# Optimization experiments

Hardware: AMD Instinct MI355X
Metric: run time of the kernel (lower is better)

## Reference

```python
import jax, jax.numpy as jnp
import numpy as np

N, E, IN_DIM, HID = 100000, 1000000, 128, 64


def setup_inputs() -> dict:
    key = jax.random.key(0)
    ks = jax.random.split(key, 9)
    x = jax.random.normal(ks[0], (N, IN_DIM), dtype=jnp.float32)
    edge_index = jax.random.randint(ks[1], (2, E), 0, N, dtype=jnp.int32)
    edge_weight = jax.random.uniform(ks[2], (E,), dtype=jnp.float32)
    # GCNConv / Linear parameters (glorot-ish scaling)
    W1 = jax.random.normal(ks[3], (IN_DIM, HID), dtype=jnp.float32) / np.sqrt(IN_DIM)
    b1 = jnp.zeros((HID,), jnp.float32)
    W2 = jax.random.normal(ks[4], (HID, HID), dtype=jnp.float32) / np.sqrt(HID)
    b2 = jnp.zeros((HID,), jnp.float32)
    Wl = jax.random.normal(ks[5], (HID, 1), dtype=jnp.float32) / np.sqrt(HID)
    bl = jnp.zeros((1,), jnp.float32)
    return {"x": x, "edge_index": edge_index, "edge_weight": edge_weight,
            "W1": W1, "b1": b1, "W2": W2, "b2": b2, "Wl": Wl, "bl": bl}


def _propagate(h, src, dst, norm, num_nodes):
    # gather neighbor features, weight by norm, scatter-add to destinations
    msg = h[src] * norm[:, None]  # [E+N, HID]
    return jax.ops.segment_sum(msg, dst, num_segments=num_nodes)


def reference(x, edge_index, edge_weight, W1, b1, W2, b2, Wl, bl):
    n = x.shape[0]
    loop = jnp.arange(n, dtype=edge_index.dtype)
    # add self-loops with weight 1 (PyG GCNConv default)
    src = jnp.concatenate([edge_index[0], loop])
    dst = jnp.concatenate([edge_index[1], loop])
    ew = jnp.concatenate([edge_weight, jnp.ones((n,), x.dtype)])
    # symmetric normalization: D^-1/2 A D^-1/2
    deg = jax.ops.segment_sum(ew, dst, num_segments=n)
    dinv = jnp.where(deg > 0, jax.lax.rsqrt(deg), 0.0)
    norm = dinv[src] * ew * dinv[dst]  # [E+N]

    h = _propagate(x @ W1, src, dst, norm, n) + b1
    h = jax.nn.relu(h)  # dropout is identity in eval mode
    h = _propagate(h @ W2, src, dst, norm, n) + b2
    h = jax.nn.relu(h)
    return (h @ Wl + bl).squeeze(-1)  # [N]
```

## Files before the change

### kernel.cpp

```cpp
#include <hip/hip_runtime.h>

#define IN_DIM 128
#define HID    64
#define SCAN_B 256

typedef __attribute__((ext_vector_type(4))) _Float16 f16x4;
typedef __attribute__((ext_vector_type(8))) _Float16 f16x8;
typedef __attribute__((ext_vector_type(4))) float    f32x4;

__global__ void k_prep_w(const float* __restrict__ W1, const float* __restrict__ W2,
                         _Float16* __restrict__ W1T, _Float16* __restrict__ W2T) {
    int i = blockIdx.x * blockDim.x + threadIdx.x;
    if (i < IN_DIM * HID) { int k = i >> 6, c = i & 63; W1T[c * IN_DIM + k] = (_Float16)W1[i]; }
    if (i < HID * HID)    { int k = i >> 6, c = i & 63; W2T[c * HID + k]    = (_Float16)W2[i]; }
}

__global__ void k_hist_rank(const int* __restrict__ dst, int* __restrict__ counts,
                            int* __restrict__ rank, int e) {
    int i = blockIdx.x * blockDim.x + threadIdx.x;
    if (i < e) rank[i] = atomicAdd(&counts[dst[i]], 1);
}

__global__ __launch_bounds__(SCAN_B) void k_scan1(int* __restrict__ data,
                                                  int* __restrict__ blockSums, int n) {
    __shared__ int s[SCAN_B];
    int tid = threadIdx.x;
    int gid = blockIdx.x * SCAN_B + tid;
    int v = (gid < n) ? data[gid] : 0;
    s[tid] = v;
    __syncthreads();
    for (int off = 1; off < SCAN_B; off <<= 1) {
        int t = (tid >= off) ? s[tid - off] : 0;
        __syncthreads();
        s[tid] += t;
        __syncthreads();
    }
    if (gid < n) data[gid] = s[tid] - v;
    if (tid == SCAN_B - 1) blockSums[blockIdx.x] = s[tid];
}

__global__ __launch_bounds__(512) void k_scan2(int* __restrict__ blockSums, int nb) {
    __shared__ int s[512];
    int tid = threadIdx.x;
    int v = (tid < nb) ? blockSums[tid] : 0;
    s[tid] = v;
    __syncthreads();
    for (int off = 1; off < 512; off <<= 1) {
        int t = (tid >= off) ? s[tid - off] : 0;
        __syncthreads();
        s[tid] += t;
        __syncthreads();
    }
    if (tid < nb) blockSums[tid] = s[tid] - v;
}

__global__ __launch_bounds__(SCAN_B) void k_scan3(int* __restrict__ data,
                                                  const int* __restrict__ blockSums,
                                                  int n, int e) {
    int gid = blockIdx.x * SCAN_B + threadIdx.x;
    if (gid < n) {
        data[gid] += blockSums[blockIdx.x];
        if (gid == n - 1) data[n] = e;
    }
}

__global__ void k_scatter(const int* __restrict__ src, const int* __restrict__ dst,
                          const float* __restrict__ ew, const int* __restrict__ rank,
                          const int* __restrict__ rowOff, int2* __restrict__ sedge, int e) {
    int i = blockIdx.x * blockDim.x + threadIdx.x;
    if (i >= e) return;
    int pos = rowOff[dst[i]] + rank[i];
    sedge[pos] = make_int2(src[i], __float_as_int(ew[i]));
}

__global__ void k_deg_dinv(const int* __restrict__ rowOff, const int2* __restrict__ sedge,
                           float* __restrict__ dinv, int n) {
    int v = blockIdx.x * blockDim.x + threadIdx.x;
    if (v >= n) return;
    int s = rowOff[v], t = rowOff[v + 1];
    float a = 1.0f;
    for (int j = s; j < t; ++j) a += __int_as_float(sedge[j].y);
    dinv[v] = rsqrtf(a);
}


__global__ __launch_bounds__(256) void k_gemm1(const float* __restrict__ x,
                                               const _Float16* __restrict__ W1T,
                                               const float* __restrict__ dinv,
                                               _Float16* __restrict__ h0, int n) {
    __shared__ _Float16 sX[4][16 * IN_DIM];
    int tid  = threadIdx.x;
    int wave = tid >> 6, lane = tid & 63;
    int row0 = blockIdx.x * 64 + wave * 16;
    int col  = lane & 15, kg = lane >> 4;

    f16x8 bfrag[4][4];
    #pragma unroll
    for (int ks = 0; ks < 4; ++ks)
        #pragma unroll
        for (int ct = 0; ct < 4; ++ct)
            bfrag[ks][ct] = *(const f16x8*)(W1T + (ct * 16 + col) * IN_DIM + ks * 32 + kg * 8);

    _Float16* myX = sX[wave];
    #pragma unroll
    for (int it = 0; it < 8; ++it) {
        int idx = it * 64 + lane;
        int r = idx >> 5, c4 = idx & 31;
        int grow = row0 + r;
        float4 v = make_float4(0.f, 0.f, 0.f, 0.f);
        if (grow < n) v = ((const float4*)x)[(size_t)grow * 32 + c4];
        f16x4 h; h.x = (_Float16)v.x; h.y = (_Float16)v.y; h.z = (_Float16)v.z; h.w = (_Float16)v.w;
        int off = (r * 256 + c4 * 8) ^ ((r & 7) << 4);
        *(f16x4*)((char*)myX + off) = h;
    }
    __syncthreads();

    f32x4 acc[4];
    #pragma unroll
    for (int ct = 0; ct < 4; ++ct) acc[ct] = (f32x4){0.f, 0.f, 0.f, 0.f};

    int arow = lane & 15;
    #pragma unroll
    for (int ks = 0; ks < 4; ++ks) {
        int off = (arow * 256 + kg * 16 + ks * 64) ^ ((arow & 7) << 4);
        f16x8 af = *(const f16x8*)((const char*)myX + off);
        #pragma unroll
        for (int ct = 0; ct < 4; ++ct)
            acc[ct] = __builtin_amdgcn_mfma_f32_16x16x32_f16(af, bfrag[ks][ct], acc[ct], 0, 0, 0);
    }

    int crow0 = row0 + kg * 4;
    #pragma unroll
    for (int r = 0; r < 4; ++r) {
        int gr = crow0 + r;
        if (gr < n) {
            float dv = dinv[gr];
            #pragma unroll
            for (int ct = 0; ct < 4; ++ct)
                h0[(size_t)gr * HID + ct * 16 + col] = (_Float16)(acc[ct][r] * dv);
        }
    }
}


__global__ __launch_bounds__(256) void k_gemm2(const _Float16* __restrict__ h1,
                                               const _Float16* __restrict__ W2T,
                                               const float* __restrict__ dinv,
                                               _Float16* __restrict__ h2, int n) {
    __shared__ _Float16 sX[4][16 * HID];
    int tid  = threadIdx.x;
    int wave = tid >> 6, lane = tid & 63;
    int row0 = blockIdx.x * 64 + wave * 16;
    int col  = lane & 15, kg = lane >> 4;

    f16x8 bfrag[2][4];
    #pragma unroll
    for (int ks = 0; ks < 2; ++ks)
        #pragma unroll
        for (int ct = 0; ct < 4; ++ct)
            bfrag[ks][ct] = *(const f16x8*)(W2T + (ct * 16 + col) * HID + ks * 32 + kg * 8);

    _Float16* myX = sX[wave];
    #pragma unroll
    for (int it = 0; it < 4; ++it) {
        int idx = it * 64 + lane;
        int r = idx >> 4, c4 = idx & 15;
        int grow = row0 + r;
        f16x4 h = (f16x4){0, 0, 0, 0};
        if (grow < n) h = ((const f16x4*)h1)[(size_t)grow * 16 + c4];
        int off = (r * 128 + c4 * 8) ^ ((r & 7) << 4);
        *(f16x4*)((char*)myX + off) = h;
    }
    __syncthreads();

    f32x4 acc[4];
    #pragma unroll
    for (int ct = 0; ct < 4; ++ct) acc[ct] = (f32x4){0.f, 0.f, 0.f, 0.f};

    int arow = lane & 15;
    #pragma unroll
    for (int ks = 0; ks < 2; ++ks) {
        int off = (arow * 128 + kg * 16 + ks * 64) ^ ((arow & 7) << 4);
        f16x8 af = *(const f16x8*)((const char*)myX + off);
        #pragma unroll
        for (int ct = 0; ct < 4; ++ct)
            acc[ct] = __builtin_amdgcn_mfma_f32_16x16x32_f16(af, bfrag[ks][ct], acc[ct], 0, 0, 0);
    }

    int crow0 = row0 + kg * 4;
    #pragma unroll
    for (int r = 0; r < 4; ++r) {
        int gr = crow0 + r;
        if (gr < n) {
            float dv = dinv[gr];
            #pragma unroll
            for (int ct = 0; ct < 4; ++ct)
                h2[(size_t)gr * HID + ct * 16 + col] = (_Float16)(acc[ct][r] * dv);
        }
    }
}


__global__ __launch_bounds__(256) void k_prop1(const int* __restrict__ rowOff,
                                               const int2* __restrict__ sedge,
                                               const _Float16* __restrict__ hin,
                                               const float* __restrict__ dinv,
                                               const float* __restrict__ b1,
                                               _Float16* __restrict__ hout, int n) {
    int wave = (blockIdx.x * blockDim.x + threadIdx.x) >> 6;
    int lane = threadIdx.x & 63;
    int g    = lane >> 4;
    int gl   = lane & 15;
    int node = wave * 4 + g;
    bool valid = node < n;
    int nd = valid ? node : 0;

    int start = rowOff[nd];
    int end   = valid ? rowOff[nd + 1] : start;
    float di  = dinv[nd];
    float4 bb = ((const float4*)b1)[gl];

    const _Float16* rowp = hin + (size_t)nd * HID + gl * 4;
    f16x4 sv = *(const f16x4*)rowp;
    float a0 = (float)sv.x, a1 = (float)sv.y, a2 = (float)sv.z, a3 = (float)sv.w;

    int j = start;
    for (; j + 4 <= end; j += 4) {
        int2 e0 = sedge[j], e1 = sedge[j + 1], e2 = sedge[j + 2], e3 = sedge[j + 3];
        f16x4 v0 = *(const f16x4*)(hin + (size_t)e0.x * HID + gl * 4);
        f16x4 v1 = *(const f16x4*)(hin + (size_t)e1.x * HID + gl * 4);
        f16x4 v2 = *(const f16x4*)(hin + (size_t)e2.x * HID + gl * 4);
        f16x4 v3 = *(const f16x4*)(hin + (size_t)e3.x * HID + gl * 4);
        float w0 = __int_as_float(e0.y), w1 = __int_as_float(e1.y);
        float w2 = __int_as_float(e2.y), w3 = __int_as_float(e3.y);
        a0 = fmaf((float)v0.x, w0, a0); a1 = fmaf((float)v0.y, w0, a1);
        a2 = fmaf((float)v0.z, w0, a2); a3 = fmaf((float)v0.w, w0, a3);
        a0 = fmaf((float)v1.x, w1, a0); a1 = fmaf((float)v1.y, w1, a1);
        a2 = fmaf((float)v1.z, w1, a2); a3 = fmaf((float)v1.w, w1, a3);
        a0 = fmaf((float)v2.x, w2, a0); a1 = fmaf((float)v2.y, w2, a1);
        a2 = fmaf((float)v2.z, w2, a2); a3 = fmaf((float)v2.w, w2, a3);
        a0 = fmaf((float)v3.x, w3, a0); a1 = fmaf((float)v3.y, w3, a1);
        a2 = fmaf((float)v3.z, w3, a2); a3 = fmaf((float)v3.w, w3, a3);
    }
    if (j < end) {
        #pragma unroll
        for (int k = 0; k < 4; ++k) {
            int idx = j + k;
            int cl  = idx < end ? idx : j;
            int2 ed = sedge[cl];
            float w = idx < end ? __int_as_float(ed.y) : 0.0f;
            f16x4 v = *(const f16x4*)(hin + (size_t)ed.x * HID + gl * 4);
            a0 = fmaf((float)v.x, w, a0); a1 = fmaf((float)v.y, w, a1);
            a2 = fmaf((float)v.z, w, a2); a3 = fmaf((float)v.w, w, a3);
        }
    }

    if (valid) {
        f16x4 o;
        o.x = (_Float16)fmaxf(fmaf(a0, di, bb.x), 0.0f);
        o.y = (_Float16)fmaxf(fmaf(a1, di, bb.y), 0.0f);
        o.z = (_Float16)fmaxf(fmaf(a2, di, bb.z), 0.0f);
        o.w = (_Float16)fmaxf(fmaf(a3, di, bb.w), 0.0f);
        *(f16x4*)(hout + (size_t)node * HID + gl * 4) = o;
    }
}

__global__ __launch_bounds__(256) void k_prop2_final(const int* __restrict__ rowOff,
                                                     const int2* __restrict__ sedge,
                                                     const _Float16* __restrict__ hin,
                                                     const float* __restrict__ dinv,
                                                     const float* __restrict__ b2,
                                                     const float* __restrict__ Wl,
                                                     const float* __restrict__ bl,
                                                     float* __restrict__ out, int n) {
    int wave = (blockIdx.x * blockDim.x + threadIdx.x) >> 6;
    int lane = threadIdx.x & 63;
    int g    = lane >> 4;
    int gl   = lane & 15;
    int node = wave * 4 + g;
    bool valid = node < n;
    int nd = valid ? node : 0;

    int start = rowOff[nd];
    int end   = valid ? rowOff[nd + 1] : start;
    float di  = dinv[nd];
    float4 bb = ((const float4*)b2)[gl];
    float4 wl = ((const float4*)Wl)[gl];

    const _Float16* rowp = hin + (size_t)nd * HID + gl * 4;
    f16x4 sv = *(const f16x4*)rowp;
    float a0 = (float)sv.x, a1 = (float)sv.y, a2 = (float)sv.z, a3 = (float)sv.w;

    int j = start;
    for (; j + 4 <= end; j += 4) {
        int2 e0 = sedge[j], e1 = sedge[j + 1], e2 = sedge[j + 2], e3 = sedge[j + 3];
        f16x4 v0 = *(const f16x4*)(hin + (size_t)e0.x * HID + gl * 4);
        f16x4 v1 = *(const f16x4*)(hin + (size_t)e1.x * HID + gl * 4);
        f16x4 v2 = *(const f16x4*)(hin + (size_t)e2.x * HID + gl * 4);
        f16x4 v3 = *(const f16x4*)(hin + (size_t)e3.x * HID + gl * 4);
        float w0 = __int_as_float(e0.y), w1 = __int_as_float(e1.y);
        float w2 = __int_as_float(e2.y), w3 = __int_as_float(e3.y);
        a0 = fmaf((float)v0.x, w0, a0); a1 = fmaf((float)v0.y, w0, a1);
        a2 = fmaf((float)v0.z, w0, a2); a3 = fmaf((float)v0.w, w0, a3);
        a0 = fmaf((float)v1.x, w1, a0); a1 = fmaf((float)v1.y, w1, a1);
        a2 = fmaf((float)v1.z, w1, a2); a3 = fmaf((float)v1.w, w1, a3);
        a0 = fmaf((float)v2.x, w2, a0); a1 = fmaf((float)v2.y, w2, a1);
        a2 = fmaf((float)v2.z, w2, a2); a3 = fmaf((float)v2.w, w2, a3);
        a0 = fmaf((float)v3.x, w3, a0); a1 = fmaf((float)v3.y, w3, a1);
        a2 = fmaf((float)v3.z, w3, a2); a3 = fmaf((float)v3.w, w3, a3);
    }
    if (j < end) {
        #pragma unroll
        for (int k = 0; k < 4; ++k) {
            int idx = j + k;
            int cl  = idx < end ? idx : j;
            int2 ed = sedge[cl];
            float w = idx < end ? __int_as_float(ed.y) : 0.0f;
            f16x4 v = *(const f16x4*)(hin + (size_t)ed.x * HID + gl * 4);
            a0 = fmaf((float)v.x, w, a0); a1 = fmaf((float)v.y, w, a1);
            a2 = fmaf((float)v.z, w, a2); a3 = fmaf((float)v.w, w, a3);
        }
    }

    float r0 = fmaxf(fmaf(a0, di, bb.x), 0.0f);
    float r1 = fmaxf(fmaf(a1, di, bb.y), 0.0f);
    float r2 = fmaxf(fmaf(a2, di, bb.z), 0.0f);
    float r3 = fmaxf(fmaf(a3, di, bb.w), 0.0f);
    float v = r0 * wl.x + r1 * wl.y + r2 * wl.z + r3 * wl.w;
    #pragma unroll
    for (int off = 1; off < 16; off <<= 1)
        v += __shfl_xor(v, off);
    if (valid && gl == 0) out[node] = v + bl[0];
}


static inline char* align16(char* p) {
    return (char*)(((uintptr_t)p + 15) & ~(uintptr_t)15);
}

extern "C" void kernel_launch(void* const* d_in, const int* in_sizes, int n_in,
                              void* d_out, int out_size, void* d_ws, size_t ws_size,
                              hipStream_t stream) {
    const float* x   = (const float*)d_in[0];
    const int*   ei  = (const int*)d_in[1];
    const float* ew  = (const float*)d_in[2];
    const float* W1  = (const float*)d_in[3];
    const float* b1  = (const float*)d_in[4];
    const float* W2  = (const float*)d_in[5];
    const float* b2  = (const float*)d_in[6];
    const float* Wl  = (const float*)d_in[7];
    const float* bl  = (const float*)d_in[8];

    const int n = in_sizes[0] / IN_DIM;
    const int e = in_sizes[2];
    const int* src = ei;
    const int* dst = ei + e;

    float* out = (float*)d_out;
    const int B256 = 256;
    const int nScanBlocks = (n + SCAN_B - 1) / SCAN_B;

    char* p = (char*)d_ws;
    int2*     sedge   = (int2*)p;             p += (size_t)e * 8;
    float*    dinv    = (float*)p;            p += (size_t)n * 4;
    int*      offsets = (int*)p;              p += ((size_t)n + 1) * 4;
    p = align16(p);
    int*      bsums   = (int*)p;              p += 512 * 4;
    int*      rank    = (int*)p;              p += (size_t)e * 4;
    _Float16* W1T     = (_Float16*)p;         p += IN_DIM * HID * 2;
    _Float16* W2T     = (_Float16*)p;         p += HID * HID * 2;
    p = align16(p);
    _Float16* A       = (_Float16*)p;         p += (size_t)n * HID * 2;
    _Float16* B       = (_Float16*)p;         p += (size_t)n * HID * 2;

    k_prep_w<<<(IN_DIM * HID + B256 - 1) / B256, B256, 0, stream>>>(W1, W2, W1T, W2T);

    hipMemsetAsync(offsets, 0, ((size_t)n + 1) * 4, stream);

    k_hist_rank<<<(e + B256 - 1) / B256, B256, 0, stream>>>(dst, offsets, rank, e);

    k_scan1<<<nScanBlocks, SCAN_B, 0, stream>>>(offsets, bsums, n);
    k_scan2<<<1, 512, 0, stream>>>(bsums, nScanBlocks);
    k_scan3<<<nScanBlocks, SCAN_B, 0, stream>>>(offsets, bsums, n, e);

    k_scatter<<<(e + B256 - 1) / B256, B256, 0, stream>>>(src, dst, ew, rank,
                                                         offsets, sedge, e);

    k_deg_dinv<<<(n + B256 - 1) / B256, B256, 0, stream>>>(offsets, sedge, dinv, n);

    const int gemmBlocks = (n + 63) / 64;
    const int propBlocks = (n + 15) / 16;

    k_gemm1<<<gemmBlocks, B256, 0, stream>>>(x, W1T, dinv, A, n);
    k_prop1<<<propBlocks, B256, 0, stream>>>(offsets, sedge, A, dinv, b1, B, n);

    k_gemm2<<<gemmBlocks, B256, 0, stream>>>(B, W2T, dinv, A, n);
    k_prop2_final<<<propBlocks, B256, 0, stream>>>(offsets, sedge, A, dinv,
                                                   b2, Wl, bl, out, n);
}
```

Baseline: 193.2 us.

## Stripe degree histogram atomics and widen propagation gathers to 16-byte loads

The per-destination histogram is split into 16 stripes chosen by wavefront index, which spreads atomic contention across separate counters. A new per-node stripe scan and a fix-up pass turn these counts into per-stripe base offsets used by the scatter. Separately, both propagation kernels now assign 8 lanes per node with f16x8 loads instead of 16 lanes with f16x4, putting 8 nodes in each wave. The stripes cost extra memset, scan and write traffic of 16 ints per node and an extra kernel launch. The wider per-lane accumulators raise register use.

```diff
diff --git a/kernel.cpp b/kernel.cpp
--- a/kernel.cpp
+++ b/kernel.cpp
@@ -3,6 +3,7 @@
 #define IN_DIM 128
 #define HID    64
 #define SCAN_B 256
+#define NSTRIPE 16
 
 typedef __attribute__((ext_vector_type(4))) _Float16 f16x4;
 typedef __attribute__((ext_vector_type(8))) _Float16 f16x8;
@@ -15,10 +16,26 @@
     if (i < HID * HID)    { int k = i >> 6, c = i & 63; W2T[c * HID + k]    = (_Float16)W2[i]; }
 }
 
-__global__ void k_hist_rank(const int* __restrict__ dst, int* __restrict__ counts,
-                            int* __restrict__ rank, int e) {
+__global__ void k_hist_rank(const int* __restrict__ dst, int* __restrict__ counts_s,
+                            int* __restrict__ rank, int n, int e) {
     int i = blockIdx.x * blockDim.x + threadIdx.x;
-    if (i < e) rank[i] = atomicAdd(&counts[dst[i]], 1);
+    if (i < e) {
+        int k = (i >> 6) & (NSTRIPE - 1);
+        rank[i] = atomicAdd(&counts_s[k * n + dst[i]], 1);
+    }
+}
+
+__global__ void k_stripe_scan(const int* __restrict__ counts_s, int* __restrict__ P,
+                              int* __restrict__ offsets, int n) {
+    int v = blockIdx.x * blockDim.x + threadIdx.x;
+    if (v >= n) return;
+    int acc = 0;
+    int pv[NSTRIPE];
+    #pragma unroll
+    for (int k = 0; k < NSTRIPE; ++k) { pv[k] = acc; acc += counts_s[k * n + v]; }
+    #pragma unroll
+    for (int k = 0; k < NSTRIPE; ++k) P[v * NSTRIPE + k] = pv[k];
+    offsets[v] = acc;
 }
 
 __global__ __launch_bounds__(SCAN_B) void k_scan1(int* __restrict__ data,
@@ -54,22 +71,26 @@
     if (tid < nb) blockSums[tid] = s[tid] - v;
 }
 
-__global__ __launch_bounds__(SCAN_B) void k_scan3(int* __restrict__ data,
-                                                  const int* __restrict__ blockSums,
-                                                  int n, int e) {
+__global__ __launch_bounds__(SCAN_B) void k_scan3_fix(int* __restrict__ data,
+                                                      const int* __restrict__ blockSums,
+                                                      int* __restrict__ P, int n, int e) {
     int gid = blockIdx.x * SCAN_B + threadIdx.x;
     if (gid < n) {
-        data[gid] += blockSums[blockIdx.x];
+        int off = data[gid] + blockSums[blockIdx.x];
+        data[gid] = off;
+        #pragma unroll
+        for (int k = 0; k < NSTRIPE; ++k) P[gid * NSTRIPE + k] += off;
         if (gid == n - 1) data[n] = e;
     }
 }
 
 __global__ void k_scatter(const int* __restrict__ src, const int* __restrict__ dst,
                           const float* __restrict__ ew, const int* __restrict__ rank,
-                          const int* __restrict__ rowOff, int2* __restrict__ sedge, int e) {
+                          const int* __restrict__ P, int2* __restrict__ sedge, int e) {
     int i = blockIdx.x * blockDim.x + threadIdx.x;
     if (i >= e) return;
-    int pos = rowOff[dst[i]] + rank[i];
+    int k = (i >> 6) & (NSTRIPE - 1);
+    int pos = P[dst[i] * NSTRIPE + k] + rank[i];
     sedge[pos] = make_int2(src[i], __float_as_int(ew[i]));
 }
 
@@ -209,38 +230,40 @@
                                                _Float16* __restrict__ hout, int n) {
     int wave = (blockIdx.x * blockDim.x + threadIdx.x) >> 6;
     int lane = threadIdx.x & 63;
-    int g    = lane >> 4;
-    int gl   = lane & 15;
-    int node = wave * 4 + g;
+    int g    = lane >> 3;
+    int gl   = lane & 7;
+    int node = wave * 8 + g;
     bool valid = node < n;
     int nd = valid ? node : 0;
 
     int start = rowOff[nd];
     int end   = valid ? rowOff[nd + 1] : start;
     float di  = dinv[nd];
-    float4 bb = ((const float4*)b1)[gl];
-
-    const _Float16* rowp = hin + (size_t)nd * HID + gl * 4;
-    f16x4 sv = *(const f16x4*)rowp;
-    float a0 = (float)sv.x, a1 = (float)sv.y, a2 = (float)sv.z, a3 = (float)sv.w;
+    float4 bbA = ((const float4*)b1)[gl * 2];
+    float4 bbB = ((const float4*)b1)[gl * 2 + 1];
+
+    f16x8 sv = *(const f16x8*)(hin + (size_t)nd * HID + gl * 8);
+    float a[8];
+    #pragma unroll
+    for (int t = 0; t < 8; ++t) a[t] = (float)sv[t];
 
     int j = start;
     for (; j + 4 <= end; j += 4) {
         int2 e0 = sedge[j], e1 = sedge[j + 1], e2 = sedge[j + 2], e3 = sedge[j + 3];
-        f16x4 v0 = *(const f16x4*)(hin + (size_t)e0.x * HID + gl * 4);
-        f16x4 v1 = *(const f16x4*)(hin + (size_t)e1.x * HID + gl * 4);
-        f16x4 v2 = *(const f16x4*)(hin + (size_t)e2.x * HID + gl * 4);
-        f16x4 v3 = *(const f16x4*)(hin + (size_t)e3.x * HID + gl * 4);
+        f16x8 v0 = *(const f16x8*)(hin + (size_t)e0.x * HID + gl * 8);
+        f16x8 v1 = *(const f16x8*)(hin + (size_t)e1.x * HID + gl * 8);
+        f16x8 v2 = *(const f16x8*)(hin + (size_t)e2.x * HID + gl * 8);
+        f16x8 v3 = *(const f16x8*)(hin + (size_t)e3.x * HID + gl * 8);
         float w0 = __int_as_float(e0.y), w1 = __int_as_float(e1.y);
         float w2 = __int_as_float(e2.y), w3 = __int_as_float(e3.y);
-        a0 = fmaf((float)v0.x, w0, a0); a1 = fmaf((float)v0.y, w0, a1);
-        a2 = fmaf((float)v0.z, w0, a2); a3 = fmaf((float)v0.w, w0, a3);
-        a0 = fmaf((float)v1.x, w1, a0); a1 = fmaf((float)v1.y, w1, a1);
-        a2 = fmaf((float)v1.z, w1, a2); a3 = fmaf((float)v1.w, w1, a3);
-        a0 = fmaf((float)v2.x, w2, a0); a1 = fmaf((float)v2.y, w2, a1);
-        a2 = fmaf((float)v2.z, w2, a2); a3 = fmaf((float)v2.w, w2, a3);
-        a0 = fmaf((float)v3.x, w3, a0); a1 = fmaf((float)v3.y, w3, a1);
-        a2 = fmaf((float)v3.z, w3, a2); a3 = fmaf((float)v3.w, w3, a3);
+        #pragma unroll
+        for (int t = 0; t < 8; ++t) a[t] = fmaf((float)v0[t], w0, a[t]);
+        #pragma unroll
+        for (int t = 0; t < 8; ++t) a[t] = fmaf((float)v1[t], w1, a[t]);
+        #pragma unroll
+        for (int t = 0; t < 8; ++t) a[t] = fmaf((float)v2[t], w2, a[t]);
+        #pragma unroll
+        for (int t = 0; t < 8; ++t) a[t] = fmaf((float)v3[t], w3, a[t]);
     }
     if (j < end) {
         #pragma unroll
@@ -249,19 +272,23 @@
             int cl  = idx < end ? idx : j;
             int2 ed = sedge[cl];
             float w = idx < end ? __int_as_float(ed.y) : 0.0f;
-            f16x4 v = *(const f16x4*)(hin + (size_t)ed.x * HID + gl * 4);
-            a0 = fmaf((float)v.x, w, a0); a1 = fmaf((float)v.y, w, a1);
-            a2 = fmaf((float)v.z, w, a2); a3 = fmaf((float)v.w, w, a3);
+            f16x8 v = *(const f16x8*)(hin + (size_t)ed.x * HID + gl * 8);
+            #pragma unroll
+            for (int t = 0; t < 8; ++t) a[t] = fmaf((float)v[t], w, a[t]);
         }
     }
 
     if (valid) {
-        f16x4 o;
-        o.x = (_Float16)fmaxf(fmaf(a0, di, bb.x), 0.0f);
-        o.y = (_Float16)fmaxf(fmaf(a1, di, bb.y), 0.0f);
-        o.z = (_Float16)fmaxf(fmaf(a2, di, bb.z), 0.0f);
-        o.w = (_Float16)fmaxf(fmaf(a3, di, bb.w), 0.0f);
-        *(f16x4*)(hout + (size_t)node * HID + gl * 4) = o;
+        f16x8 o;
+        o[0] = (_Float16)fmaxf(fmaf(a[0], di, bbA.x), 0.0f);
+        o[1] = (_Float16)fmaxf(fmaf(a[1], di, bbA.y), 0.0f);
+        o[2] = (_Float16)fmaxf(fmaf(a[2], di, bbA.z), 0.0f);
+        o[3] = (_Float16)fmaxf(fmaf(a[3], di, bbA.w), 0.0f);
+        o[4] = (_Float16)fmaxf(fmaf(a[4], di, bbB.x), 0.0f);
+        o[5] = (_Float16)fmaxf(fmaf(a[5], di, bbB.y), 0.0f);
+        o[6] = (_Float16)fmaxf(fmaf(a[6], di, bbB.z), 0.0f);
+        o[7] = (_Float16)fmaxf(fmaf(a[7], di, bbB.w), 0.0f);
+        *(f16x8*)(hout + (size_t)node * HID + gl * 8) = o;
     }
 }
 
@@ -275,39 +302,42 @@
                                                      float* __restrict__ out, int n) {
     int wave = (blockIdx.x * blockDim.x + threadIdx.x) >> 6;
     int lane = threadIdx.x & 63;
-    int g    = lane >> 4;
-    int gl   = lane & 15;
-    int node = wave * 4 + g;
+    int g    = lane >> 3;
+    int gl   = lane & 7;
+    int node = wave * 8 + g;
     bool valid = node < n;
     int nd = valid ? node : 0;
 
     int start = rowOff[nd];
     int end   = valid ? rowOff[nd + 1] : start;
     float di  = dinv[nd];
-    float4 bb = ((const float4*)b2)[gl];
-    float4 wl = ((const float4*)Wl)[gl];
-
-    const _Float16* rowp = hin + (size_t)nd * HID + gl * 4;
-    f16x4 sv = *(const f16x4*)rowp;
-    float a0 = (float)sv.x, a1 = (float)sv.y, a2 = (float)sv.z, a3 = (float)sv.w;
+    float4 bbA = ((const float4*)b2)[gl * 2];
+    float4 bbB = ((const float4*)b2)[gl * 2 + 1];
+    float4 wlA = ((const float4*)Wl)[gl * 2];
+    float4 wlB = ((const float4*)Wl)[gl * 2 + 1];
+
+    f16x8 sv = *(const f16x8*)(hin + (size_t)nd * HID + gl * 8);
+    float a[8];
+    #pragma unroll
+    for (int t = 0; t < 8; ++t) a[t] = (float)sv[t];
 
     int j = start;
     for (; j + 4 <= end; j += 4) {
         int2 e0 = sedge[j], e1 = sedge[j + 1], e2 = sedge[j + 2], e3 = sedge[j + 3];
-        f16x4 v0 = *(const f16x4*)(hin + (size_t)e0.x * HID + gl * 4);
-        f16x4 v1 = *(const f16x4*)(hin + (size_t)e1.x * HID + gl * 4);
-        f16x4 v2 = *(const f16x4*)(hin + (size_t)e2.x * HID + gl * 4);
-        f16x4 v3 = *(const f16x4*)(hin + (size_t)e3.x * HID + gl * 4);
+        f16x8 v0 = *(const f16x8*)(hin + (size_t)e0.x * HID + gl * 8);
+        f16x8 v1 = *(const f16x8*)(hin + (size_t)e1.x * HID + gl * 8);
+        f16x8 v2 = *(const f16x8*)(hin + (size_t)e2.x * HID + gl * 8);
+        f16x8 v3 = *(const f16x8*)(hin + (size_t)e3.x * HID + gl * 8);
         float w0 = __int_as_float(e0.y), w1 = __int_as_float(e1.y);
         float w2 = __int_as_float(e2.y), w3 = __int_as_float(e3.y);
-        a0 = fmaf((float)v0.x, w0, a0); a1 = fmaf((float)v0.y, w0, a1);
-        a2 = fmaf((float)v0.z, w0, a2); a3 = fmaf((float)v0.w, w0, a3);
-        a0 = fmaf((float)v1.x, w1, a0); a1 = fmaf((float)v1.y, w1, a1);
-        a2 = fmaf((float)v1.z, w1, a2); a3 = fmaf((float)v1.w, w1, a3);
-        a0 = fmaf((float)v2.x, w2, a0); a1 = fmaf((float)v2.y, w2, a1);
-        a2 = fmaf((float)v2.z, w2, a2); a3 = fmaf((float)v2.w, w2, a3);
-        a0 = fmaf((float)v3.x, w3, a0); a1 = fmaf((float)v3.y, w3, a1);
-        a2 = fmaf((float)v3.z, w3, a2); a3 = fmaf((float)v3.w, w3, a3);
+        #pragma unroll
+        for (int t = 0; t < 8; ++t) a[t] = fmaf((float)v0[t], w0, a[t]);
+        #pragma unroll
+        for (int t = 0; t < 8; ++t) a[t] = fmaf((float)v1[t], w1, a[t]);
+        #pragma unroll
+        for (int t = 0; t < 8; ++t) a[t] = fmaf((float)v2[t], w2, a[t]);
+        #pragma unroll
+        for (int t = 0; t < 8; ++t) a[t] = fmaf((float)v3[t], w3, a[t]);
     }
     if (j < end) {
         #pragma unroll
@@ -316,19 +346,20 @@
             int cl  = idx < end ? idx : j;
             int2 ed = sedge[cl];
             float w = idx < end ? __int_as_float(ed.y) : 0.0f;
-            f16x4 v = *(const f16x4*)(hin + (size_t)ed.x * HID + gl * 4);
-            a0 = fmaf((float)v.x, w, a0); a1 = fmaf((float)v.y, w, a1);
-            a2 = fmaf((float)v.z, w, a2); a3 = fmaf((float)v.w, w, a3);
+            f16x8 v = *(const f16x8*)(hin + (size_t)ed.x * HID + gl * 8);
+            #pragma unroll
+            for (int t = 0; t < 8; ++t) a[t] = fmaf((float)v[t], w, a[t]);
         }
     }
 
-    float r0 = fmaxf(fmaf(a0, di, bb.x), 0.0f);
-    float r1 = fmaxf(fmaf(a1, di, bb.y), 0.0f);
-    float r2 = fmaxf(fmaf(a2, di, bb.z), 0.0f);
-    float r3 = fmaxf(fmaf(a3, di, bb.w), 0.0f);
-    float v = r0 * wl.x + r1 * wl.y + r2 * wl.z + r3 * wl.w;
-    #pragma unroll
-    for (int off = 1; off < 16; off <<= 1)
+    float bb[8] = {bbA.x, bbA.y, bbA.z, bbA.w, bbB.x, bbB.y, bbB.z, bbB.w};
+    float wl[8] = {wlA.x, wlA.y, wlA.z, wlA.w, wlB.x, wlB.y, wlB.z, wlB.w};
+    float v = 0.0f;
+    #pragma unroll
+    for (int t = 0; t < 8; ++t)
+        v += fmaxf(fmaf(a[t], di, bb[t]), 0.0f) * wl[t];
+    #pragma unroll
+    for (int off = 1; off < 8; off <<= 1)
         v += __shfl_xor(v, off);
     if (valid && gl == 0) out[node] = v + bl[0];
 }
@@ -361,35 +392,39 @@
     const int nScanBlocks = (n + SCAN_B - 1) / SCAN_B;
 
     char* p = (char*)d_ws;
-    int2*     sedge   = (int2*)p;             p += (size_t)e * 8;
-    float*    dinv    = (float*)p;            p += (size_t)n * 4;
-    int*      offsets = (int*)p;              p += ((size_t)n + 1) * 4;
+    int2*     sedge    = (int2*)p;            p += (size_t)e * 8;
+    float*    dinv     = (float*)p;           p += (size_t)n * 4;
+    int*      offsets  = (int*)p;             p += ((size_t)n + 1) * 4;
     p = align16(p);
-    int*      bsums   = (int*)p;              p += 512 * 4;
-    int*      rank    = (int*)p;              p += (size_t)e * 4;
-    _Float16* W1T     = (_Float16*)p;         p += IN_DIM * HID * 2;
-    _Float16* W2T     = (_Float16*)p;         p += HID * HID * 2;
+    int*      bsums    = (int*)p;             p += 512 * 4;
+    int*      rank     = (int*)p;             p += (size_t)e * 4;
     p = align16(p);
-    _Float16* A       = (_Float16*)p;         p += (size_t)n * HID * 2;
-    _Float16* B       = (_Float16*)p;         p += (size_t)n * HID * 2;
+    int*      counts_s = (int*)p;             p += (size_t)NSTRIPE * n * 4;
+    int*      P        = (int*)p;             p += (size_t)NSTRIPE * n * 4;
+    _Float16* W1T      = (_Float16*)p;        p += IN_DIM * HID * 2;
+    _Float16* W2T      = (_Float16*)p;        p += HID * HID * 2;
+    p = align16(p);
+    _Float16* A        = (_Float16*)p;        p += (size_t)n * HID * 2;
+    _Float16* B        = (_Float16*)p;        p += (size_t)n * HID * 2;
 
     k_prep_w<<<(IN_DIM * HID + B256 - 1) / B256, B256, 0, stream>>>(W1, W2, W1T, W2T);
 
-    hipMemsetAsync(offsets, 0, ((size_t)n + 1) * 4, stream);
-
-    k_hist_rank<<<(e + B256 - 1) / B256, B256, 0, stream>>>(dst, offsets, rank, e);
+    hipMemsetAsync(counts_s, 0, (size_t)NSTRIPE * n * 4, stream);
+
+    k_hist_rank<<<(e + B256 - 1) / B256, B256, 0, stream>>>(dst, counts_s, rank, n, e);
+
+    k_stripe_scan<<<(n + B256 - 1) / B256, B256, 0, stream>>>(counts_s, P, offsets, n);
 
     k_scan1<<<nScanBlocks, SCAN_B, 0, stream>>>(offsets, bsums, n);
     k_scan2<<<1, 512, 0, stream>>>(bsums, nScanBlocks);
-    k_scan3<<<nScanBlocks, SCAN_B, 0, stream>>>(offsets, bsums, n, e);
-
-    k_scatter<<<(e + B256 - 1) / B256, B256, 0, stream>>>(src, dst, ew, rank,
-                                                         offsets, sedge, e);
+    k_scan3_fix<<<nScanBlocks, SCAN_B, 0, stream>>>(offsets, bsums, P, n, e);
+
+    k_scatter<<<(e + B256 - 1) / B256, B256, 0, stream>>>(src, dst, ew, rank, P, sedge, e);
 
     k_deg_dinv<<<(n + B256 - 1) / B256, B256, 0, stream>>>(offsets, sedge, dinv, n);
 
     const int gemmBlocks = (n + 63) / 64;
-    const int propBlocks = (n + 15) / 16;
+    const int propBlocks = (n + 31) / 32;
 
     k_gemm1<<<gemmBlocks, B256, 0, stream>>>(x, W1T, dinv, A, n);
     k_prop1<<<propBlocks, B256, 0, stream>>>(offsets, sedge, A, dinv, b1, B, n);
```

After: 207.7 us. +7.5%, slower.
